# Optimization experiments

Measured on AMD Instinct MI355X. Metric: run time of the kernel, lower is better.

Reference implementation:

```python
import jax, jax.numpy as jnp
import numpy as np

CONSTRAINT_WEIGHT = 0.5
FOCAL_GAMMA = 2.0
EPS = 1e-8

B, G, C = 65536, 9, 9
BLK = 3  # int(sqrt(G))


def setup_inputs() -> dict:
    key = jax.random.key(0)
    k1, k2, k3 = jax.random.split(key, 3)
    logits = jax.random.normal(k1, (B, G, G, C), dtype=jnp.float32)
    targets = jax.random.randint(k2, (B, G, G), 0, 10, dtype=jnp.int64)
    puzzles = jax.random.randint(k3, (B, G, G), 0, 10, dtype=jnp.int64)
    return {"logits": logits, "targets": targets, "puzzles": puzzles}


def _sudoku_loss(logits, targets, puzzles):
    b, g, _, c = logits.shape
    mask = (puzzles == 0).astype(logits.dtype)            # [B,G,G]
    tgt = jnp.clip(targets - 1, 0, c - 1)                 # [B,G,G]

    log_probs = jax.nn.log_softmax(logits, axis=-1)       # [B,G,G,C]
    probs = jnp.exp(log_probs)

    # --- focal CE over masked (empty) cells ---
    lp_t = jnp.take_along_axis(log_probs, tgt[..., None], axis=-1)[..., 0]  # [B,G,G]
    pt = jnp.exp(lp_t)
    ce = -lp_t
    focal = (1.0 - pt) ** FOCAL_GAMMA * ce
    msum = mask.sum()
    ce_loss = (focal * mask).sum() / (msum + EPS)

    # --- constraint loss ---
    masked_probs = probs * mask[..., None]                # [B,G,G,C]
    row_sums = masked_probs.sum(axis=2)                   # [B,G,C]
    row_loss = jnp.mean((row_sums - 1.0) ** 2)
    col_sums = masked_probs.sum(axis=1)                   # [B,G,C]
    col_loss = jnp.mean((col_sums - 1.0) ** 2)
    # boxes: [B, br, r, bc, c_in, C] -> sum over the 3x3 cells of each box
    box = masked_probs.reshape(b, BLK, BLK, BLK, BLK, c)
    box_sums = box.transpose(0, 1, 3, 2, 4, 5).reshape(b, BLK * BLK, BLK * BLK, c).sum(axis=2)
    box_loss = jnp.mean((box_sums - 1.0) ** 2)

    entropy = -(probs * log_probs).sum(axis=-1)           # [B,G,G]
    entropy_loss = 0.1 * ((entropy * mask).sum() / (msum + EPS))

    top2, _ = jax.lax.top_k(probs, 2)                     # [B,G,G,2]
    gap = top2[..., 0] - top2[..., 1]
    uniqueness_loss = 0.1 * jnp.mean(jax.nn.relu(1.0 - gap))

    constraint_loss = (row_loss + col_loss + box_loss + entropy_loss + uniqueness_loss) * 0.2
    return ce_loss + CONSTRAINT_WEIGHT * constraint_loss


def reference(logits, targets, puzzles):
    return _sudoku_loss(logits, targets, puzzles)
```

## Files before the change

### kernel.cpp

```cpp
#include <hip/hip_runtime.h>

#define THREADS 256
#define PB 3
#define COLW 84

typedef float f4 __attribute__((ext_vector_type(4)));
typedef f4 f4a4 __attribute__((aligned(4)));

__global__ __launch_bounds__(THREADS) void sudoku_main(
    const float* __restrict__ logits,
    const int*   __restrict__ targets,
    const int*   __restrict__ puzzles,
    float* __restrict__ acc,
    int B)
{
  __shared__ float probT[2][PB * 9 * COLW];
  __shared__ float sred[4][5];

  const int tid  = threadIdx.x;
  const int lp   = tid / 81;
  const int cell = tid % 81;
  const bool workerA = tid < 243;
  const int cpad = 28 * (cell / 27) + (cell % 27);
  const int B81  = B * 81;
  const int numGroups = (B + PB - 1) / PB;

  const int cw   = tid >> 6;
  const int l27  = tid & 63;
  const bool workerC = (l27 < 27) && (cw < 3);
  const int ccls = l27 / 3;
  const int ck   = l27 % 3;

  float a_focal = 0.f, a_ent = 0.f, a_msk = 0.f, a_uniq = 0.f, a_sq = 0.f;

  int g0 = blockIdx.x;
  bool vA = workerA && (g0 < numGroups) && (g0 * 243 + tid < B81);
  f4 c0{}, c1{}; float c8 = 0.f; int ctg = 0, cpz = 0;
  if (vA) {
    const float* Lp = logits + (size_t)(g0 * 243 + tid) * 9;
    c0 = *(const f4a4*)Lp; c1 = *(const f4a4*)(Lp + 4); c8 = Lp[8];
    ctg = targets[g0 * 243 + tid]; cpz = puzzles[g0 * 243 + tid];
  }

  int it = 0;
  for (int g = blockIdx.x; g < numGroups; g += gridDim.x, ++it) {
    float* PT = probT[it & 1];

    if (vA) {
      float l[9];
      l[0]=c0[0]; l[1]=c0[1]; l[2]=c0[2]; l[3]=c0[3];
      l[4]=c1[0]; l[5]=c1[1]; l[6]=c1[2]; l[7]=c1[3]; l[8]=c8;
      int tg = ctg - 1; tg = tg < 0 ? 0 : (tg > 8 ? 8 : tg);

      float t1 = l[0], t2 = -3.0e38f;
#pragma unroll
      for (int i = 1; i < 9; ++i) {
        float hi = fmaxf(t1, l[i]);
        float lo = fminf(t1, l[i]);
        t1 = hi;
        t2 = fmaxf(t2, lo);
      }
      float e[9], s = 0.f, lsum = 0.f, ltg = l[0];
#pragma unroll
      for (int i = 0; i < 9; ++i) {
        float x  = l[i] - t1;
        float ei = __expf(x);
        e[i] = ei;
        s += ei;
        lsum = fmaf(ei, x, lsum);
        if (i > 0) ltg = (tg == i) ? l[i] : ltg;
      }
      float inv_s = __builtin_amdgcn_rcpf(s);
      float logs  = __logf(s);
      float lpt   = (ltg - t1) - logs;
      float pt    = __expf(lpt);
      float om    = 1.f - pt;
      float focal = om * om * (-lpt);
      float ent   = logs - lsum * inv_s;
      float gap   = (1.f - __expf(t2 - t1)) * inv_s;
      float uq    = fmaxf(0.f, 1.f - gap);
      float mk    = (cpz == 0) ? 1.f : 0.f;
      a_focal += focal * mk;
      a_ent   += ent * mk;
      a_msk   += mk;
      a_uniq  += uq;
      float pm = inv_s * mk;
#pragma unroll
      for (int i = 0; i < 9; ++i)
        PT[(lp * 9 + i) * COLW + cpad] = e[i] * pm;
    }

    const int gn = g + (int)gridDim.x;
    const bool vAn = workerA && (gn < numGroups) && (gn * 243 + tid < B81);
    f4 n0{}, n1{}; float n8 = 0.f; int ntg = 0, npz = 0;
    if (vAn) {
      const float* Lp = logits + (size_t)(gn * 243 + tid) * 9;
      n0 = *(const f4a4*)Lp; n1 = *(const f4a4*)(Lp + 4); n8 = Lp[8];
      ntg = targets[gn * 243 + tid]; npz = puzzles[gn * 243 + tid];
    }

    __syncthreads();

    if (workerC && (g * PB + cw) < B) {
      const float* base = PT + (cw * 9 + ccls) * COLW + 28 * ck;
      float vv[28];
      ((f4*)vv)[0] = *(const f4*)(base);
      ((f4*)vv)[1] = *(const f4*)(base + 4);
      ((f4*)vv)[2] = *(const f4*)(base + 8);
      ((f4*)vv)[3] = *(const f4*)(base + 12);
      ((f4*)vv)[4] = *(const f4*)(base + 16);
      ((f4*)vv)[5] = *(const f4*)(base + 20);
      ((f4*)vv)[6] = *(const f4*)(base + 24);
      float rs[3] = {0.f,0.f,0.f}, bs[3] = {0.f,0.f,0.f};
      float cs[9] = {0.f,0.f,0.f,0.f,0.f,0.f,0.f,0.f,0.f};
#pragma unroll
      for (int j = 0; j < 27; ++j) {
        float v = vv[j];
        rs[j / 9]       += v;
        cs[j % 9]       += v;
        bs[(j % 9) / 3] += v;
      }
#pragma unroll
      for (int r = 0; r < 3; ++r) {
        float d = rs[r] - 1.f; a_sq = fmaf(d, d, a_sq);
        d = bs[r] - 1.f;       a_sq = fmaf(d, d, a_sq);
      }
      float csq = 0.f;
#pragma unroll
      for (int c9 = 0; c9 < 9; ++c9) {
        float t = cs[c9] + __shfl_down(cs[c9], 1) + __shfl_down(cs[c9], 2);
        float d = t - 1.f;
        csq = fmaf(d, d, csq);
      }
      if (ck == 0) a_sq += csq;
    }

    vA = vAn; c0 = n0; c1 = n1; c8 = n8; ctg = ntg; cpz = npz;
  }

#pragma unroll
  for (int off = 32; off > 0; off >>= 1) {
    a_focal += __shfl_down(a_focal, off);
    a_ent   += __shfl_down(a_ent,   off);
    a_msk   += __shfl_down(a_msk,   off);
    a_uniq  += __shfl_down(a_uniq,  off);
    a_sq    += __shfl_down(a_sq,    off);
  }
  const int wave = tid >> 6;
  if ((tid & 63) == 0) {
    sred[wave][0] = a_focal; sred[wave][1] = a_ent; sred[wave][2] = a_msk;
    sred[wave][3] = a_uniq;  sred[wave][4] = a_sq;
  }
  __syncthreads();
  if (tid < 5) {
    float v = sred[0][tid] + sred[1][tid] + sred[2][tid] + sred[3][tid];
    atomicAdd(&acc[tid], v);
  }
}

__global__ void sudoku_finalize(const float* __restrict__ acc,
                                float* __restrict__ out, float invBG)
{
  float focal = acc[0], ent = acc[1], msum = acc[2], uniq = acc[3], sq = acc[4];
  float inv_m = 1.f / (msum + 1e-8f);
  float ce    = focal * inv_m;
  float entl  = 0.1f * ent * inv_m;
  float uql   = 0.1f * uniq * invBG;
  float rcb   = sq * invBG;
  float constraint = (rcb + entl + uql) * 0.2f;
  out[0] = ce + 0.5f * constraint;
}

extern "C" void kernel_launch(void* const* d_in, const int* in_sizes, int n_in,
                              void* d_out, int out_size, void* d_ws, size_t ws_size,
                              hipStream_t stream)
{
  (void)n_in; (void)out_size; (void)ws_size;
  const float* logits  = (const float*)d_in[0];
  const int*   targets = (const int*)d_in[1];
  const int*   puzzles = (const int*)d_in[2];
  float* out = (float*)d_out;
  float* acc = (float*)d_ws;

  const int B = in_sizes[0] / 729;
  const int numGroups = (B + PB - 1) / PB;

  hipMemsetAsync(acc, 0, 5 * sizeof(float), stream);

  int grid = numGroups < 2048 ? numGroups : 2048;
  sudoku_main<<<grid, THREADS, 0, stream>>>(logits, targets, puzzles, acc, B);

  const float invBG = 1.f / ((float)B * 81.f);
  sudoku_finalize<<<1, 1, 0, stream>>>(acc, out, invBG);
}
```

Before: 61.04 us.

## Pack probabilities as fp16 pairs in LDS and rotate constraint-sum work across waves

Stores the masked probabilities in shared memory as packed fp16 pairs, which halves LDS traffic. Row, column and box sums are now computed with packed half adds by 15 lanes of a single wave, and that wave rotates each iteration so the constraint work is spread across the waves. The global atomics and the memset are replaced by per-block partial sums that a 256-thread finalize kernel reduces. The fp16 accumulation (round toward zero) loses precision in the constraint sums, which risks tolerance failures, and the serial per-lane sums may lengthen the critical path.

```diff
diff --git a/kernel.cpp b/kernel.cpp
--- a/kernel.cpp
+++ b/kernel.cpp
@@ -2,19 +2,29 @@
 
 #define THREADS 256
 #define PB 3
+#define NPAIR 5
 #define COLW 84
+#define MAXGRID 2048
 
 typedef float f4 __attribute__((ext_vector_type(4)));
 typedef f4 f4a4 __attribute__((aligned(4)));
+typedef __fp16 h2 __attribute__((ext_vector_type(2)));
+typedef unsigned int u32;
+typedef u32 u32x4 __attribute__((ext_vector_type(4)));
+
+static __device__ __forceinline__ u32 pkrtz(float a, float b) {
+  h2 v = __builtin_amdgcn_cvt_pkrtz(a, b);
+  return __builtin_bit_cast(u32, v);
+}
 
 __global__ __launch_bounds__(THREADS) void sudoku_main(
     const float* __restrict__ logits,
     const int*   __restrict__ targets,
     const int*   __restrict__ puzzles,
-    float* __restrict__ acc,
+    float* __restrict__ partial,
     int B)
 {
-  __shared__ float probT[2][PB * 9 * COLW];
+  __shared__ u32 probT[2][PB * NPAIR * COLW];
   __shared__ float sred[4][5];
 
   const int tid  = threadIdx.x;
@@ -25,26 +35,24 @@
   const int B81  = B * 81;
   const int numGroups = (B + PB - 1) / PB;
 
-  const int cw   = tid >> 6;
-  const int l27  = tid & 63;
-  const bool workerC = (l27 < 27) && (cw < 3);
-  const int ccls = l27 / 3;
-  const int ck   = l27 % 3;
+  const int lane = tid & 63;
+  const int wv   = tid >> 6;
+  const int clp  = lane / NPAIR;
+  const int cpr  = lane % NPAIR;
 
   float a_focal = 0.f, a_ent = 0.f, a_msk = 0.f, a_uniq = 0.f, a_sq = 0.f;
 
-  int g0 = blockIdx.x;
-  bool vA = workerA && (g0 < numGroups) && (g0 * 243 + tid < B81);
+  bool vA = workerA && (blockIdx.x * 243 + tid < B81);
   f4 c0{}, c1{}; float c8 = 0.f; int ctg = 0, cpz = 0;
   if (vA) {
-    const float* Lp = logits + (size_t)(g0 * 243 + tid) * 9;
+    const float* Lp = logits + (size_t)(blockIdx.x * 243 + tid) * 9;
     c0 = *(const f4a4*)Lp; c1 = *(const f4a4*)(Lp + 4); c8 = Lp[8];
-    ctg = targets[g0 * 243 + tid]; cpz = puzzles[g0 * 243 + tid];
+    ctg = targets[blockIdx.x * 243 + tid]; cpz = puzzles[blockIdx.x * 243 + tid];
   }
 
   int it = 0;
   for (int g = blockIdx.x; g < numGroups; g += gridDim.x, ++it) {
-    float* PT = probT[it & 1];
+    u32* PT = probT[it & 1];
 
     if (vA) {
       float l[9];
@@ -57,16 +65,14 @@
       for (int i = 1; i < 9; ++i) {
         float hi = fmaxf(t1, l[i]);
         float lo = fminf(t1, l[i]);
-        t1 = hi;
-        t2 = fmaxf(t2, lo);
+        t1 = hi; t2 = fmaxf(t2, lo);
       }
       float e[9], s = 0.f, lsum = 0.f, ltg = l[0];
 #pragma unroll
       for (int i = 0; i < 9; ++i) {
         float x  = l[i] - t1;
         float ei = __expf(x);
-        e[i] = ei;
-        s += ei;
+        e[i] = ei; s += ei;
         lsum = fmaf(ei, x, lsum);
         if (i > 0) ltg = (tg == i) ? l[i] : ltg;
       }
@@ -85,9 +91,13 @@
       a_msk   += mk;
       a_uniq  += uq;
       float pm = inv_s * mk;
-#pragma unroll
-      for (int i = 0; i < 9; ++i)
-        PT[(lp * 9 + i) * COLW + cpad] = e[i] * pm;
+
+      const int wbase = lp * (NPAIR * COLW) + cpad;
+      PT[wbase + 0*COLW] = pkrtz(e[0]*pm, e[1]*pm);
+      PT[wbase + 1*COLW] = pkrtz(e[2]*pm, e[3]*pm);
+      PT[wbase + 2*COLW] = pkrtz(e[4]*pm, e[5]*pm);
+      PT[wbase + 3*COLW] = pkrtz(e[6]*pm, e[7]*pm);
+      PT[wbase + 4*COLW] = pkrtz(e[8]*pm, 0.f);
     }
 
     const int gn = g + (int)gridDim.x;
@@ -101,38 +111,38 @@
 
     __syncthreads();
 
-    if (workerC && (g * PB + cw) < B) {
-      const float* base = PT + (cw * 9 + ccls) * COLW + 28 * ck;
-      float vv[28];
-      ((f4*)vv)[0] = *(const f4*)(base);
-      ((f4*)vv)[1] = *(const f4*)(base + 4);
-      ((f4*)vv)[2] = *(const f4*)(base + 8);
-      ((f4*)vv)[3] = *(const f4*)(base + 12);
-      ((f4*)vv)[4] = *(const f4*)(base + 16);
-      ((f4*)vv)[5] = *(const f4*)(base + 20);
-      ((f4*)vv)[6] = *(const f4*)(base + 24);
-      float rs[3] = {0.f,0.f,0.f}, bs[3] = {0.f,0.f,0.f};
-      float cs[9] = {0.f,0.f,0.f,0.f,0.f,0.f,0.f,0.f,0.f};
-#pragma unroll
-      for (int j = 0; j < 27; ++j) {
-        float v = vv[j];
-        rs[j / 9]       += v;
-        cs[j % 9]       += v;
-        bs[(j % 9) / 3] += v;
-      }
-#pragma unroll
-      for (int r = 0; r < 3; ++r) {
-        float d = rs[r] - 1.f; a_sq = fmaf(d, d, a_sq);
-        d = bs[r] - 1.f;       a_sq = fmaf(d, d, a_sq);
-      }
-      float csq = 0.f;
-#pragma unroll
-      for (int c9 = 0; c9 < 9; ++c9) {
-        float t = cs[c9] + __shfl_down(cs[c9], 1) + __shfl_down(cs[c9], 2);
-        float d = t - 1.f;
-        csq = fmaf(d, d, csq);
-      }
-      if (ck == 0) a_sq += csq;
+    if (wv == (it & 3) && lane < PB * NPAIR && (g * PB + clp) < B) {
+      const u32* base = PT + (clp * NPAIR + cpr) * COLW;
+      h2 hz; hz[0] = (__fp16)0.f; hz[1] = (__fp16)0.f;
+      h2 rs[9], cs[9], bs[9];
+#pragma unroll
+      for (int u = 0; u < 9; ++u) { rs[u] = hz; cs[u] = hz; bs[u] = hz; }
+#pragma unroll
+      for (int b = 0; b < 3; ++b) {
+        u32x4 w[7];
+#pragma unroll
+        for (int q = 0; q < 7; ++q) w[q] = *(const u32x4*)(base + b * 28 + q * 4);
+#pragma unroll
+        for (int j = 0; j < 27; ++j) {
+          h2 v = __builtin_bit_cast(h2, w[j >> 2][j & 3]);
+          rs[3 * b + j / 9]       += v;
+          cs[j % 9]               += v;
+          bs[3 * b + (j % 9) / 3] += v;
+        }
+      }
+      const float hiw = (cpr == NPAIR - 1) ? 0.f : 1.f;
+      float sq = 0.f;
+#pragma unroll
+      for (int u = 0; u < 9; ++u) {
+        float x;
+        x = (float)rs[u][0] - 1.f; sq = fmaf(x, x, sq);
+        x = (float)cs[u][0] - 1.f; sq = fmaf(x, x, sq);
+        x = (float)bs[u][0] - 1.f; sq = fmaf(x, x, sq);
+        x = (float)rs[u][1] - 1.f; sq = fmaf(hiw * x, x, sq);
+        x = (float)cs[u][1] - 1.f; sq = fmaf(hiw * x, x, sq);
+        x = (float)bs[u][1] - 1.f; sq = fmaf(hiw * x, x, sq);
+      }
+      a_sq += sq;
     }
 
     vA = vAn; c0 = n0; c1 = n1; c8 = n8; ctg = ntg; cpz = npz;
@@ -146,29 +156,53 @@
     a_uniq  += __shfl_down(a_uniq,  off);
     a_sq    += __shfl_down(a_sq,    off);
   }
-  const int wave = tid >> 6;
-  if ((tid & 63) == 0) {
-    sred[wave][0] = a_focal; sred[wave][1] = a_ent; sred[wave][2] = a_msk;
-    sred[wave][3] = a_uniq;  sred[wave][4] = a_sq;
+  if (lane == 0) {
+    sred[wv][0] = a_focal; sred[wv][1] = a_ent; sred[wv][2] = a_msk;
+    sred[wv][3] = a_uniq;  sred[wv][4] = a_sq;
   }
   __syncthreads();
   if (tid < 5) {
     float v = sred[0][tid] + sred[1][tid] + sred[2][tid] + sred[3][tid];
-    atomicAdd(&acc[tid], v);
-  }
-}
-
-__global__ void sudoku_finalize(const float* __restrict__ acc,
-                                float* __restrict__ out, float invBG)
+    partial[(size_t)blockIdx.x * 8 + tid] = v;
+  }
+}
+
+__global__ __launch_bounds__(256) void sudoku_finalize(
+    const float* __restrict__ partial, float* __restrict__ out,
+    int nblk, float invBG)
 {
-  float focal = acc[0], ent = acc[1], msum = acc[2], uniq = acc[3], sq = acc[4];
-  float inv_m = 1.f / (msum + 1e-8f);
-  float ce    = focal * inv_m;
-  float entl  = 0.1f * ent * inv_m;
-  float uql   = 0.1f * uniq * invBG;
-  float rcb   = sq * invBG;
-  float constraint = (rcb + entl + uql) * 0.2f;
-  out[0] = ce + 0.5f * constraint;
+  __shared__ float sb[4][5];
+  const int tid = threadIdx.x;
+  float s[5] = {0.f, 0.f, 0.f, 0.f, 0.f};
+  for (int b = tid; b < nblk; b += 256) {
+    const float* row = partial + (size_t)b * 8;
+#pragma unroll
+    for (int u = 0; u < 5; ++u) s[u] += row[u];
+  }
+#pragma unroll
+  for (int off = 32; off > 0; off >>= 1)
+#pragma unroll
+    for (int u = 0; u < 5; ++u) s[u] += __shfl_down(s[u], off);
+  const int wv = tid >> 6, lane = tid & 63;
+  if (lane == 0) {
+#pragma unroll
+    for (int u = 0; u < 5; ++u) sb[wv][u] = s[u];
+  }
+  __syncthreads();
+  if (tid == 0) {
+    float focal = sb[0][0] + sb[1][0] + sb[2][0] + sb[3][0];
+    float ent   = sb[0][1] + sb[1][1] + sb[2][1] + sb[3][1];
+    float msum  = sb[0][2] + sb[1][2] + sb[2][2] + sb[3][2];
+    float uniq  = sb[0][3] + sb[1][3] + sb[2][3] + sb[3][3];
+    float sq    = sb[0][4] + sb[1][4] + sb[2][4] + sb[3][4];
+    float inv_m = 1.f / (msum + 1e-8f);
+    float ce    = focal * inv_m;
+    float entl  = 0.1f * ent * inv_m;
+    float uql   = 0.1f * uniq * invBG;
+    float rcb   = sq * invBG;
+    float constraint = (rcb + entl + uql) * 0.2f;
+    out[0] = ce + 0.5f * constraint;
+  }
 }
 
 extern "C" void kernel_launch(void* const* d_in, const int* in_sizes, int n_in,
@@ -180,16 +214,14 @@
   const int*   targets = (const int*)d_in[1];
   const int*   puzzles = (const int*)d_in[2];
   float* out = (float*)d_out;
-  float* acc = (float*)d_ws;
+  float* partial = (float*)d_ws;
 
   const int B = in_sizes[0] / 729;
   const int numGroups = (B + PB - 1) / PB;
-
-  hipMemsetAsync(acc, 0, 5 * sizeof(float), stream);
-
-  int grid = numGroups < 2048 ? numGroups : 2048;
-  sudoku_main<<<grid, THREADS, 0, stream>>>(logits, targets, puzzles, acc, B);
+  int grid = numGroups < MAXGRID ? numGroups : MAXGRID;
+
+  sudoku_main<<<grid, THREADS, 0, stream>>>(logits, targets, puzzles, partial, B);
 
   const float invBG = 1.f / ((float)B * 81.f);
-  sudoku_finalize<<<1, 1, 0, stream>>>(acc, out, invBG);
-}
+  sudoku_finalize<<<1, 256, 0, stream>>>(partial, out, grid, invBG);
+}
```

After: 58.30 us. 1.05x faster.
